# Kernel tuning notes

Measured on AMD Instinct MI355X. Metric: run time of the kernel, lower is better.

The kernel has to match this reference:

```python
import jax, jax.numpy as jnp
import numpy as np

N_NODES = 100000
N_EDGES = 6400000
N_ORDERS = 4
EPO = N_EDGES // N_ORDERS  # edges per order
K = 10


def setup_inputs() -> dict:
    key = jax.random.key(0)
    ks = jax.random.split(key, 7)
    x = jax.random.normal(ks[0], (N_NODES, K), dtype=jnp.float32)
    w_mp = jax.random.normal(ks[1], (K, 2 * K), dtype=jnp.float32) * (1.0 / np.sqrt(2 * K))
    b_mp = jax.random.normal(ks[2], (K,), dtype=jnp.float32) * 0.01
    w_out = jax.random.normal(ks[3], (K, K), dtype=jnp.float32) * (1.0 / np.sqrt(K))
    b_out = jax.random.normal(ks[4], (K,), dtype=jnp.float32) * 0.01
    edge_index = jax.random.randint(ks[5], (2, N_EDGES), 0, N_NODES, dtype=jnp.int64)
    orders = jax.random.randint(ks[6], (N_ORDERS, EPO), 0, N_EDGES, dtype=jnp.int64)
    return {"x": x, "w_mp": w_mp, "b_mp": b_mp, "w_out": w_out,
            "b_out": b_out, "edge_index": edge_index, "orders": orders}


def reference(x, w_mp, b_mp, w_out, b_out, edge_index, orders):
    n = x.shape[0]

    def step(h, order_idx):
        ei = edge_index[:, order_idx]            # [2, EPO] edges of this order
        # torch code swaps rows [1,0] before propagate, so in PyG terms:
        # source j = original row 1, target i = original row 0
        dst = ei[0]
        src = ei[1]
        x_i = h[dst]                             # [EPO, K]
        x_j = h[src]                             # [EPO, K]
        msg_in = jnp.concatenate([x_i, x_j - x_i], axis=1)   # [EPO, 2K]
        msg = msg_in @ w_mp.T + b_mp             # [EPO, K]
        aggr = jax.ops.segment_sum(msg, dst, num_segments=n)  # scatter-add
        return aggr + h, None                    # update(): aggr_out + x

    h, _ = jax.lax.scan(step, x, orders)
    return h @ w_out.T + b_out
```

## Files before the change

kernel.cpp:

```cpp
#include <hip/hip_runtime.h>

#define BLK 256
#define WBITS 13
#define W1CAP 9216
#define STCAP 4608
#define MAXNW 1024
#define MAXK2 2048
#define MAXNBD 512
#define OVFN 65536
#define IPTA 32
#define NSL 18
#define SENT 0xFFFFFFFFu

__global__ void k_init_h(const float* __restrict__ x, float* __restrict__ h, int n) {
    int total = n * 16;
    int gs = gridDim.x * blockDim.x;
    for (int i = blockIdx.x * blockDim.x + threadIdx.x; i < total; i += gs) {
        int row = i >> 4, col = i & 15;
        h[i] = (col < 10) ? x[row * 10 + col] : 0.0f;
    }
}

__global__ __launch_bounds__(512) void k_win(const int* __restrict__ orders,
                                             int total, int epo, int NW,
                                             int* __restrict__ gcnt1,
                                             unsigned* __restrict__ recs1,
                                             int* __restrict__ ovf1_cnt,
                                             unsigned* __restrict__ ovf1) {
    __shared__ int bcnt[MAXNW];
    __shared__ int gbase[MAXNW];
    int t = threadIdx.x;
    for (int i = t; i < NW; i += 512) bcnt[i] = 0;
    __syncthreads();

    size_t base = (size_t)blockIdx.x * (512 * IPTA);
    int st0 = (int)(base / (size_t)epo);
    size_t b1 = (size_t)(st0 + 1) * (size_t)epo;

    unsigned recr[IPTA]; int rr[IPTA];
    #pragma unroll
    for (int q = 0; q < IPTA; ++q) {
        size_t g = base + (size_t)q * 512 + t;
        recr[q] = SENT; rr[q] = 0;
        if (g < (size_t)total) {
            int idx = orders[g];
            int st = (g >= b1) ? (st0 + 1) : st0;
            recr[q] = ((unsigned)st << 23) | (unsigned)idx;
            rr[q] = atomicAdd(&bcnt[idx >> WBITS], 1);
        }
    }
    __syncthreads();
    for (int k = t; k < NW; k += 512) {
        int c = bcnt[k];
        gbase[k] = c ? atomicAdd(&gcnt1[k], c) : 0;
    }
    __syncthreads();
    #pragma unroll
    for (int q = 0; q < IPTA; ++q) {
        if (recr[q] != SENT) {
            int idx = (int)(recr[q] & 0x7FFFFFu);
            int key = idx >> WBITS;
            int pos = gbase[key] + rr[q];
            if (pos < W1CAP)
                recs1[(size_t)key * W1CAP + pos] = recr[q];
            else {
                int o = atomicAdd(ovf1_cnt, 1);
                if (o < OVFN) ovf1[o] = recr[q];
            }
        }
    }
}

__global__ __launch_bounds__(512) void k_bsort(const int* __restrict__ ei, int ne,
                                               const int* __restrict__ gcnt1,
                                               const unsigned* __restrict__ recs1,
                                               int NW, int NBD, int K2,
                                               unsigned* __restrict__ recs2,
                                               int* __restrict__ blk_offs) {
    __shared__ unsigned srt[W1CAP];
    __shared__ int cnt2[MAXK2];
    __shared__ int lofs[MAXK2 + 1];
    __shared__ int sc[512];
    int t = threadIdx.x;
    for (int i = t; i < K2; i += 512) cnt2[i] = 0;
    __syncthreads();

    int w = blockIdx.x;
    int c = gcnt1[w]; if (c > W1CAP) c = W1CAP;
    const unsigned* strm = recs1 + (size_t)w * W1CAP;

    int recr[NSL];
    #pragma unroll
    for (int q = 0; q < NSL; ++q) {
        int r = q * 512 + t;
        recr[q] = (r < c) ? (int)strm[r] : -1;
    }
    int dv[NSL];
    #pragma unroll
    for (int q = 0; q < NSL; ++q)
        dv[q] = (recr[q] >= 0) ? ei[recr[q] & 0x7FFFFF] : 0;
    unsigned meta[NSL];
    #pragma unroll
    for (int q = 0; q < NSL; ++q) {
        meta[q] = SENT;
        if (recr[q] >= 0) {
            int st = (int)(((unsigned)recr[q]) >> 23);
            int key = st * NBD + (dv[q] >> 8);
            int rk = atomicAdd(&cnt2[key], 1);
            meta[q] = ((unsigned)dv[q] << 14) | (unsigned)rk;
        }
    }
    __syncthreads();

    {
        int v[4]; int sum = 0;
        #pragma unroll
        for (int i = 0; i < 4; ++i) {
            int k = t * 4 + i;
            v[i] = (k < K2) ? cnt2[k] : 0;
            sum += v[i];
        }
        sc[t] = sum;
        __syncthreads();
        for (int off = 1; off < 512; off <<= 1) {
            int u = (t >= off) ? sc[t - off] : 0;
            __syncthreads();
            sc[t] += u;
            __syncthreads();
        }
        int run = sc[t] - sum;
        #pragma unroll
        for (int i = 0; i < 4; ++i) {
            int k = t * 4 + i;
            if (k <= K2) lofs[k] = run;
            run += v[i];
        }
        if (t == 511) lofs[K2] = sc[511];
    }
    __syncthreads();

    #pragma unroll
    for (int q = 0; q < NSL; ++q) {
        if (meta[q] != SENT) {
            int idx = recr[q] & 0x7FFFFF;
            int st  = (int)(((unsigned)recr[q]) >> 23);
            int s = ei[(size_t)ne + idx];
            int d = (int)(meta[q] >> 14);
            int rk = (int)(meta[q] & 0x3FFFu);
            int key = st * NBD + (d >> 8);
            srt[lofs[key] + rk] = ((unsigned)(d & 255) << 20) | (unsigned)s;
        }
    }
    __syncthreads();

    unsigned* dst = recs2 + (size_t)w * W1CAP;
    for (int r = t; r < c; r += 512) dst[r] = srt[r];
    int* bo = blk_offs + (size_t)w * (K2 + 1);
    for (int k = t; k <= K2; k += 512) bo[k] = lofs[k];
}

template<bool FINAL>
__global__ __launch_bounds__(512) void k_agg3(const float* __restrict__ h_cur,
                                              float* __restrict__ h_next,
                                              const int* __restrict__ blk_offs,
                                              const unsigned* __restrict__ recs2,
                                              int NW, int K2, int NBD, int st,
                                              const float* __restrict__ w_mp,
                                              const float* __restrict__ b_mp,
                                              const float* __restrict__ w_out,
                                              const float* __restrict__ b_out,
                                              float* __restrict__ out, int n,
                                              int* __restrict__ ovf2_cnt,
                                              int2* __restrict__ ovf2) {
    __shared__ unsigned stage[STCAP];
    __shared__ unsigned srt[STCAP];
    __shared__ int cnts[256];
    __shared__ int sc[256];
    __shared__ int offs[257];
    __shared__ int cursor;
    __shared__ float part[256 * 10];
    __shared__ float Wa[100], Wb[100], Bm[10];
    __shared__ float Wo[100], Bo[10];
    int t = threadIdx.x;
    if (t < 100) {
        int k = t / 10, j = t - k * 10;
        float w1 = w_mp[k * 20 + j];
        float w2 = w_mp[k * 20 + 10 + j];
        Wa[t] = w1 - w2; Wb[t] = w2;
        if (FINAL) Wo[t] = w_out[t];
    }
    if (t < 10) { Bm[t] = b_mp[t]; if (FINAL) Bo[t] = b_out[t]; }
    if (t < 256) cnts[t] = 0;
    if (t == 0) cursor = 0;
    __syncthreads();

    int bkt = blockIdx.x;
    int key = st * NBD + bkt;

    for (int b = t; b < NW; b += 512) {
        const int* bo = blk_offs + (size_t)b * (K2 + 1) + key;
        int o0 = bo[0], o1 = bo[1];
        int len = o1 - o0;
        if (len > 0) {
            int base = atomicAdd(&cursor, len);
            const unsigned* src = recs2 + (size_t)b * W1CAP + o0;
            for (int i = 0; i < len; ++i) {
                unsigned rec = src[i];
                int pos = base + i;
                if (pos < STCAP) {
                    stage[pos] = rec;
                    atomicAdd(&cnts[rec >> 20], 1);
                } else {
                    int o = atomicAdd(ovf2_cnt, 1);
                    if (o < OVFN)
                        ovf2[o] = make_int2((st << 18) | (bkt * 256 + (int)(rec >> 20)),
                                            (int)(rec & 0xFFFFFu));
                }
            }
        }
    }
    __syncthreads();
    int T = cursor; if (T > STCAP) T = STCAP;

    if (t < 256) sc[t] = cnts[t];
    __syncthreads();
    for (int off = 1; off < 256; off <<= 1) {
        int v = (t < 256 && t >= off) ? sc[t - off] : 0;
        __syncthreads();
        if (t < 256) sc[t] += v;
        __syncthreads();
    }
    if (t < 256) offs[t + 1] = sc[t];
    if (t == 0) offs[0] = 0;
    __syncthreads();
    if (t < 256) cnts[t] = offs[t];
    __syncthreads();

    for (int r = t; r < T; r += 512) {
        unsigned rec = stage[r];
        int pos = atomicAdd(&cnts[rec >> 20], 1);
        srt[pos] = rec;
    }
    __syncthreads();

    int node = t & 255, half = t >> 8;
    int b0 = offs[node], m = offs[node + 1] - b0;
    float S[10] = {0,0,0,0,0,0,0,0,0,0};
    for (int p = b0 + half; p < b0 + m; p += 2) {
        int s = (int)(srt[p] & 0xFFFFFu);
        const float* pj = h_cur + (size_t)s * 16;
        float4 a0 = *(const float4*)(pj);
        float4 a1 = *(const float4*)(pj + 4);
        float2 a2 = *(const float2*)(pj + 8);
        S[0] += a0.x; S[1] += a0.y; S[2] += a0.z; S[3] += a0.w;
        S[4] += a1.x; S[5] += a1.y; S[6] += a1.z; S[7] += a1.w;
        S[8] += a2.x; S[9] += a2.y;
    }
    if (half == 1) {
        #pragma unroll
        for (int j = 0; j < 10; ++j) part[node * 10 + j] = S[j];
    }
    __syncthreads();
    if (half == 0) {
        int i = bkt * 256 + node;
        if (i < n) {
            #pragma unroll
            for (int j = 0; j < 10; ++j) S[j] += part[node * 10 + j];
            const float* pi = h_cur + (size_t)i * 16;
            float4 x0 = *(const float4*)(pi);
            float4 x1 = *(const float4*)(pi + 4);
            float2 x2 = *(const float2*)(pi + 8);
            float xi[10] = {x0.x, x0.y, x0.z, x0.w, x1.x, x1.y, x1.z, x1.w, x2.x, x2.y};
            float deg = (float)m;
            float o[10];
            #pragma unroll
            for (int k = 0; k < 10; ++k) {
                float ma = Bm[k];
                float mb = 0.0f;
                #pragma unroll
                for (int j = 0; j < 10; ++j) {
                    ma += Wa[k * 10 + j] * xi[j];
                    mb += Wb[k * 10 + j] * S[j];
                }
                o[k] = xi[k] + deg * ma + mb;
            }
            if (FINAL) {
                float q2[10];
                #pragma unroll
                for (int k = 0; k < 10; ++k) {
                    float m2 = Bo[k];
                    #pragma unroll
                    for (int j = 0; j < 10; ++j) m2 += Wo[k * 10 + j] * o[j];
                    q2[k] = m2;
                }
                float* po = out + (size_t)i * 10;
                *(float2*)(po)     = make_float2(q2[0], q2[1]);
                *(float2*)(po + 2) = make_float2(q2[2], q2[3]);
                *(float2*)(po + 4) = make_float2(q2[4], q2[5]);
                *(float2*)(po + 6) = make_float2(q2[6], q2[7]);
                *(float2*)(po + 8) = make_float2(q2[8], q2[9]);
            } else {
                float* po = h_next + (size_t)i * 16;
                *(float4*)(po)     = make_float4(o[0], o[1], o[2], o[3]);
                *(float4*)(po + 4) = make_float4(o[4], o[5], o[6], o[7]);
                *(float2*)(po + 8) = make_float2(o[8], o[9]);
            }
        }
    }
}

__global__ void k_fix(const float* __restrict__ h_cur, float* __restrict__ h_next,
                      const int* __restrict__ ei, int ne,
                      const int* __restrict__ ovf1_cnt, const unsigned* __restrict__ ovf1,
                      const int* __restrict__ ovf2_cnt, const int2* __restrict__ ovf2,
                      const float* __restrict__ w_mp, const float* __restrict__ b_mp,
                      int st) {
    __shared__ float Wa[100], Wb[100], Bm[10];
    int t = threadIdx.x;
    if (t < 100) {
        int k = t / 10, j = t - k * 10;
        float w1 = w_mp[k * 20 + j];
        float w2 = w_mp[k * 20 + 10 + j];
        Wa[t] = w1 - w2; Wb[t] = w2;
    }
    if (t < 10) Bm[t] = b_mp[t];
    __syncthreads();
    int c1 = *ovf1_cnt; if (c1 > OVFN) c1 = OVFN;
    int c2 = *ovf2_cnt; if (c2 > OVFN) c2 = OVFN;
    int gs = gridDim.x * blockDim.x;
    for (int i = blockIdx.x * blockDim.x + t; i < c1 + c2; i += gs) {
        int d, s;
        if (i < c1) {
            unsigned v = ovf1[i];
            if ((int)(v >> 23) != st) continue;
            int idx = (int)(v & 0x7FFFFFu);
            d = ei[idx]; s = ei[(size_t)ne + idx];
        } else {
            int2 p = ovf2[i - c1];
            if ((p.x >> 18) != st) continue;
            d = p.x & 0x3FFFF; s = p.y;
        }
        const float* pi = h_cur + (size_t)d * 16;
        const float* pj = h_cur + (size_t)s * 16;
        float xi[10], xj[10];
        #pragma unroll
        for (int j = 0; j < 10; ++j) { xi[j] = pi[j]; xj[j] = pj[j]; }
        float* po = h_next + (size_t)d * 16;
        #pragma unroll
        for (int k = 0; k < 10; ++k) {
            float m = Bm[k];
            #pragma unroll
            for (int j = 0; j < 10; ++j) m += Wa[k * 10 + j] * xi[j] + Wb[k * 10 + j] * xj[j];
            atomicAdd(po + k, m);
        }
    }
}

__global__ void k_fix_final(const float* __restrict__ h_cur, float* __restrict__ out,
                            const int* __restrict__ ei, int ne,
                            const int* __restrict__ ovf1_cnt, const unsigned* __restrict__ ovf1,
                            const int* __restrict__ ovf2_cnt, const int2* __restrict__ ovf2,
                            const float* __restrict__ w_mp, const float* __restrict__ b_mp,
                            const float* __restrict__ w_out, int st) {
    __shared__ float Wa[100], Wb[100], Bm[10], Wo[100];
    int t = threadIdx.x;
    if (t < 100) {
        int k = t / 10, j = t - k * 10;
        float w1 = w_mp[k * 20 + j];
        float w2 = w_mp[k * 20 + 10 + j];
        Wa[t] = w1 - w2; Wb[t] = w2;
        Wo[t] = w_out[t];
    }
    if (t < 10) Bm[t] = b_mp[t];
    __syncthreads();
    int c1 = *ovf1_cnt; if (c1 > OVFN) c1 = OVFN;
    int c2 = *ovf2_cnt; if (c2 > OVFN) c2 = OVFN;
    int gs = gridDim.x * blockDim.x;
    for (int i = blockIdx.x * blockDim.x + t; i < c1 + c2; i += gs) {
        int d, s;
        if (i < c1) {
            unsigned v = ovf1[i];
            if ((int)(v >> 23) != st) continue;
            int idx = (int)(v & 0x7FFFFFu);
            d = ei[idx]; s = ei[(size_t)ne + idx];
        } else {
            int2 p = ovf2[i - c1];
            if ((p.x >> 18) != st) continue;
            d = p.x & 0x3FFFF; s = p.y;
        }
        const float* pi = h_cur + (size_t)d * 16;
        const float* pj = h_cur + (size_t)s * 16;
        float xi[10], xj[10];
        #pragma unroll
        for (int j = 0; j < 10; ++j) { xi[j] = pi[j]; xj[j] = pj[j]; }
        float dm[10];
        #pragma unroll
        for (int k = 0; k < 10; ++k) {
            float m = Bm[k];
            #pragma unroll
            for (int j = 0; j < 10; ++j) m += Wa[k * 10 + j] * xi[j] + Wb[k * 10 + j] * xj[j];
            dm[k] = m;
        }
        float* po = out + (size_t)d * 10;
        #pragma unroll
        for (int q = 0; q < 10; ++q) {
            float m = 0.0f;
            #pragma unroll
            for (int k = 0; k < 10; ++k) m += Wo[q * 10 + k] * dm[k];
            atomicAdd(po + q, m);
        }
    }
}


__global__ void k_init10(const float* __restrict__ x, float* __restrict__ h, int n10) {
    int gs = gridDim.x * blockDim.x;
    for (int i = blockIdx.x * blockDim.x + threadIdx.x; i < n10; i += gs) h[i] = x[i];
}
__global__ void k_copy4(const float4* __restrict__ src, float4* __restrict__ dst, int n4) {
    int gs = gridDim.x * blockDim.x;
    for (int i = blockIdx.x * blockDim.x + threadIdx.x; i < n4; i += gs) dst[i] = src[i];
}
__global__ void k_edge_step10(const float* __restrict__ h_cur, float* __restrict__ h_next,
                              const int* __restrict__ edge_index, const int* __restrict__ order,
                              const float* __restrict__ w_mp, const float* __restrict__ b_mp,
                              int epo, int ne) {
    __shared__ float Wc[200]; __shared__ float Bc[10];
    int t = threadIdx.x;
    if (t < 200) {
        int k = t / 20, j = t - k * 20;
        float w = w_mp[t];
        Wc[t] = (j < 10) ? (w - w_mp[k * 20 + j + 10]) : w;
    }
    if (t < 10) Bc[t] = b_mp[t];
    __syncthreads();
    int gs = gridDim.x * blockDim.x;
    for (int e = blockIdx.x * blockDim.x + t; e < epo; e += gs) {
        int idx = order[e];
        int dst = edge_index[idx];
        int src = edge_index[(size_t)ne + idx];
        const float* pi = h_cur + (size_t)dst * 10;
        const float* pj = h_cur + (size_t)src * 10;
        float xi[10], xj[10];
        #pragma unroll
        for (int j = 0; j < 10; ++j) { xi[j] = pi[j]; xj[j] = pj[j]; }
        float* po = h_next + (size_t)dst * 10;
        #pragma unroll
        for (int k = 0; k < 10; ++k) {
            float m = Bc[k];
            #pragma unroll
            for (int j = 0; j < 10; ++j) m += Wc[k * 20 + j] * xi[j] + Wc[k * 20 + 10 + j] * xj[j];
            atomicAdd(po + k, m);
        }
    }
}
__global__ void k_out10(const float* __restrict__ h, const float* __restrict__ w_out,
                        const float* __restrict__ b_out, float* __restrict__ out, int n) {
    __shared__ float W[100]; __shared__ float B[10];
    int t = threadIdx.x;
    if (t < 100) W[t] = w_out[t];
    if (t < 10)  B[t] = b_out[t];
    __syncthreads();
    int gs = gridDim.x * blockDim.x;
    for (int i = blockIdx.x * blockDim.x + t; i < n; i += gs) {
        float xi[10];
        #pragma unroll
        for (int j = 0; j < 10; ++j) xi[j] = h[(size_t)i * 10 + j];
        #pragma unroll
        for (int k = 0; k < 10; ++k) {
            float m = B[k];
            #pragma unroll
            for (int j = 0; j < 10; ++j) m += W[k * 10 + j] * xi[j];
            out[(size_t)i * 10 + k] = m;
        }
    }
}


extern "C" void kernel_launch(void* const* d_in, const int* in_sizes, int n_in,
                              void* d_out, int out_size, void* d_ws, size_t ws_size,
                              hipStream_t stream) {
    const float* x      = (const float*)d_in[0];
    const float* w_mp   = (const float*)d_in[1];
    const float* b_mp   = (const float*)d_in[2];
    const float* w_out  = (const float*)d_in[3];
    const float* b_out  = (const float*)d_in[4];
    const int*   edge_i = (const int*)d_in[5];
    const int*   orders = (const int*)d_in[6];

    int n  = in_sizes[0] / 10;
    int ne = in_sizes[5] / 2;
    const int n_orders = 4;
    int epo = in_sizes[6] / n_orders;
    int total = n_orders * epo;

    float* out = (float*)d_out;

    int NBD = (n + 255) >> 8;
    int NW  = (ne + (1 << WBITS) - 1) >> WBITS;
    int K2  = 4 * NBD;

    size_t off_hA    = 0;
    size_t off_hB    = off_hA + (size_t)n * 16;
    size_t off_recs1 = off_hB + (size_t)n * 16;
    size_t off_recs2 = off_recs1 + (size_t)NW * W1CAP;
    size_t off_boffs = off_recs2 + (size_t)NW * W1CAP;
    size_t off_ovf2  = off_boffs + (size_t)NW * (K2 + 1);
    if (off_ovf2 & 1) off_ovf2++;
    size_t off_ovf1  = off_ovf2 + (size_t)2 * OVFN;
    size_t off_gcnt1 = off_ovf1 + OVFN;
    size_t off_cnts  = off_gcnt1 + NW;
    size_t need      = (off_cnts + 2) * 4;

    bool ok = (ws_size >= need) && (NW <= MAXNW) && (NBD <= MAXNBD) &&
              (K2 <= MAXK2) && (ne <= (1 << 23)) && (n < (1 << 17));

    if (!ok) {
        float* hA = (float*)d_ws;
        float* hB = hA + (size_t)n * 10;
        int n10 = n * 10;
        hipLaunchKernelGGL(k_init10, dim3(min((n10 + BLK - 1) / BLK, 2048)), dim3(BLK), 0, stream,
                           x, hA, n10);
        int n4 = n10 / 4;
        float* cur = hA; float* nxt = hB;
        int gb_edge = min((epo + BLK - 1) / BLK, 6400);
        for (int s = 0; s < n_orders; ++s) {
            hipLaunchKernelGGL(k_copy4, dim3(min((n4 + BLK - 1) / BLK, 2048)), dim3(BLK), 0, stream,
                               (const float4*)cur, (float4*)nxt, n4);
            hipLaunchKernelGGL(k_edge_step10, dim3(gb_edge), dim3(BLK), 0, stream,
                               cur, nxt, edge_i, orders + (size_t)s * epo, w_mp, b_mp, epo, ne);
            float* t2 = cur; cur = nxt; nxt = t2;
        }
        hipLaunchKernelGGL(k_out10, dim3(min((n + BLK - 1) / BLK, 2048)), dim3(BLK), 0, stream,
                           cur, w_out, b_out, out, n);
        return;
    }

    float*    hA      = (float*)d_ws;
    float*    hB      = (float*)d_ws + off_hB;
    unsigned* recs1   = (unsigned*)d_ws + off_recs1;
    unsigned* recs2   = (unsigned*)d_ws + off_recs2;
    int*      boffs   = (int*)d_ws + off_boffs;
    int2*     ovf2    = (int2*)((int*)d_ws + off_ovf2);
    unsigned* ovf1    = (unsigned*)d_ws + off_ovf1;
    int*      gcnt1   = (int*)d_ws + off_gcnt1;
    int*      ovfcnts = (int*)d_ws + off_cnts;

    hipMemsetAsync(gcnt1, 0, ((size_t)NW + 2) * sizeof(int), stream);

    int gb_init = min((n * 16 + BLK - 1) / BLK, 2048);
    hipLaunchKernelGGL(k_init_h, dim3(gb_init), dim3(BLK), 0, stream, x, hA, n);

    int gbA = (total + 512 * IPTA - 1) / (512 * IPTA);
    hipLaunchKernelGGL(k_win, dim3(gbA), dim3(512), 0, stream,
                       orders, total, epo, NW, gcnt1, recs1, ovfcnts + 0, ovf1);

    hipLaunchKernelGGL(k_bsort, dim3(NW), dim3(512), 0, stream,
                       edge_i, ne, gcnt1, recs1, NW, NBD, K2, recs2, boffs);

    float* cur = hA; float* nxt = hB;
    for (int s = 0; s < n_orders; ++s) {
        bool fin = (s == n_orders - 1);
        if (fin) {
            hipLaunchKernelGGL((k_agg3<true>), dim3(NBD), dim3(512), 0, stream,
                               cur, nxt, boffs, recs2, NW, K2, NBD, s,
                               w_mp, b_mp, w_out, b_out, out, n,
                               ovfcnts + 1, ovf2);
            hipLaunchKernelGGL(k_fix_final, dim3(8), dim3(256), 0, stream,
                               cur, out, edge_i, ne,
                               ovfcnts + 0, ovf1, ovfcnts + 1, ovf2,
                               w_mp, b_mp, w_out, s);
        } else {
            hipLaunchKernelGGL((k_agg3<false>), dim3(NBD), dim3(512), 0, stream,
                               cur, nxt, boffs, recs2, NW, K2, NBD, s,
                               w_mp, b_mp, w_out, b_out, out, n,
                               ovfcnts + 1, ovf2);
            hipLaunchKernelGGL(k_fix, dim3(8), dim3(256), 0, stream,
                               cur, nxt, edge_i, ne,
                               ovfcnts + 0, ovf1, ovfcnts + 1, ovf2,
                               w_mp, b_mp, s);
            float* t2 = cur; cur = nxt; nxt = t2;
        }
    }
}
```

Baseline: 287.0 us.

## Replace global-atomic window binning with per-tile local sort and wave-parallel gather

The first binning pass now sorts each 8192-record tile by window in shared memory and writes contiguous runs plus per-tile offsets, replacing scattered writes driven by global atomics. The bucket-sort kernel gathers its window's runs from all tiles through a staging buffer. Both it and the aggregation kernel copy runs with whole wavefronts instead of one thread per run. This removes global atomic contention and serial per-thread copy loops, at the cost of an extra offset table and a gather stage.

```diff
diff --git a/kernel.cpp b/kernel.cpp
--- a/kernel.cpp
+++ b/kernel.cpp
@@ -2,14 +2,16 @@
 
 #define BLK 256
 #define WBITS 13
+#define TILEW 8192
+#define IPTW 16
 #define W1CAP 9216
+#define NSL 18
 #define STCAP 4608
 #define MAXNW 1024
+#define MAXNWB 1024
 #define MAXK2 2048
 #define MAXNBD 512
 #define OVFN 65536
-#define IPTA 32
-#define NSL 18
 #define SENT 0xFFFFFFFFu
 
 __global__ void k_init_h(const float* __restrict__ x, float* __restrict__ h, int n) {
@@ -21,79 +23,120 @@
     }
 }
 
-__global__ __launch_bounds__(512) void k_win(const int* __restrict__ orders,
-                                             int total, int epo, int NW,
-                                             int* __restrict__ gcnt1,
-                                             unsigned* __restrict__ recs1,
-                                             int* __restrict__ ovf1_cnt,
-                                             unsigned* __restrict__ ovf1) {
+__global__ __launch_bounds__(512) void k_win2(const int* __restrict__ orders,
+                                              int total, int epo, int NW,
+                                              unsigned* __restrict__ recs1,
+                                              int* __restrict__ woffs) {
+    __shared__ unsigned srt[TILEW];
     __shared__ int bcnt[MAXNW];
-    __shared__ int gbase[MAXNW];
+    __shared__ int lofs[MAXNW + 1];
+    __shared__ int sc[512];
     int t = threadIdx.x;
     for (int i = t; i < NW; i += 512) bcnt[i] = 0;
     __syncthreads();
 
-    size_t base = (size_t)blockIdx.x * (512 * IPTA);
+    int b = blockIdx.x;
+    size_t base = (size_t)b * TILEW;
+    int lim = (int)((size_t)total - base < TILEW ? (size_t)total - base : TILEW);
     int st0 = (int)(base / (size_t)epo);
-    size_t b1 = (size_t)(st0 + 1) * (size_t)epo;
-
-    unsigned recr[IPTA]; int rr[IPTA];
+    size_t bnd = (size_t)(st0 + 1) * (size_t)epo;
+
+    unsigned recr[IPTW]; int rr[IPTW];
     #pragma unroll
-    for (int q = 0; q < IPTA; ++q) {
-        size_t g = base + (size_t)q * 512 + t;
+    for (int q = 0; q < IPTW; ++q) {
+        int e = q * 512 + t;
         recr[q] = SENT; rr[q] = 0;
-        if (g < (size_t)total) {
+        if (e < lim) {
+            size_t g = base + e;
             int idx = orders[g];
-            int st = (g >= b1) ? (st0 + 1) : st0;
+            int st = (g >= bnd) ? (st0 + 1) : st0;
             recr[q] = ((unsigned)st << 23) | (unsigned)idx;
             rr[q] = atomicAdd(&bcnt[idx >> WBITS], 1);
         }
     }
     __syncthreads();
-    for (int k = t; k < NW; k += 512) {
-        int c = bcnt[k];
-        gbase[k] = c ? atomicAdd(&gcnt1[k], c) : 0;
+    {
+        int k0 = 2 * t;
+        int v0 = (k0 < NW) ? bcnt[k0] : 0;
+        int v1 = (k0 + 1 < NW) ? bcnt[k0 + 1] : 0;
+        int sum = v0 + v1;
+        sc[t] = sum;
+        __syncthreads();
+        for (int off = 1; off < 512; off <<= 1) {
+            int u = (t >= off) ? sc[t - off] : 0;
+            __syncthreads();
+            sc[t] += u;
+            __syncthreads();
+        }
+        int run = sc[t] - sum;
+        if (k0 <= NW) lofs[k0] = run;
+        if (k0 + 1 <= NW) lofs[k0 + 1] = run + v0;
     }
     __syncthreads();
     #pragma unroll
-    for (int q = 0; q < IPTA; ++q) {
+    for (int q = 0; q < IPTW; ++q) {
         if (recr[q] != SENT) {
             int idx = (int)(recr[q] & 0x7FFFFFu);
-            int key = idx >> WBITS;
-            int pos = gbase[key] + rr[q];
-            if (pos < W1CAP)
-                recs1[(size_t)key * W1CAP + pos] = recr[q];
-            else {
-                int o = atomicAdd(ovf1_cnt, 1);
-                if (o < OVFN) ovf1[o] = recr[q];
-            }
-        }
-    }
+            srt[lofs[idx >> WBITS] + rr[q]] = recr[q];
+        }
+    }
+    __syncthreads();
+    unsigned* dst = recs1 + base;
+    for (int r = t; r < lim; r += 512) dst[r] = srt[r];
+    int* bo = woffs + (size_t)b * (NW + 1);
+    for (int k = t; k <= NW; k += 512) bo[k] = lofs[k];
 }
 
 __global__ __launch_bounds__(512) void k_bsort(const int* __restrict__ ei, int ne,
-                                               const int* __restrict__ gcnt1,
                                                const unsigned* __restrict__ recs1,
-                                               int NW, int NBD, int K2,
+                                               const int* __restrict__ woffs,
+                                               int NWB, int NW, int NBD, int K2,
                                                unsigned* __restrict__ recs2,
-                                               int* __restrict__ blk_offs) {
-    __shared__ unsigned srt[W1CAP];
+                                               int* __restrict__ boffs,
+                                               int* __restrict__ ovf1_cnt,
+                                               unsigned* __restrict__ ovf1) {
+    __shared__ unsigned stage[W1CAP];
     __shared__ int cnt2[MAXK2];
     __shared__ int lofs[MAXK2 + 1];
     __shared__ int sc[512];
+    __shared__ int so0[MAXNWB];
+    __shared__ int slen[MAXNWB];
+    __shared__ int cursor;
     int t = threadIdx.x;
+    int w = blockIdx.x;
     for (int i = t; i < K2; i += 512) cnt2[i] = 0;
-    __syncthreads();
-
-    int w = blockIdx.x;
-    int c = gcnt1[w]; if (c > W1CAP) c = W1CAP;
-    const unsigned* strm = recs1 + (size_t)w * W1CAP;
+    if (t == 0) cursor = 0;
+    for (int b = t; b < NWB; b += 512) {
+        const int* bo = woffs + (size_t)b * (NW + 1) + w;
+        int o0 = bo[0];
+        so0[b] = o0;
+        slen[b] = bo[1] - o0;
+    }
+    __syncthreads();
+
+    int lane = t & 63, wid = t >> 6;
+    for (int b = wid; b < NWB; b += 8) {
+        int len = slen[b];
+        if (len > 0) {
+            int bs = 0;
+            if (lane == 0) bs = atomicAdd(&cursor, len);
+            bs = __shfl(bs, 0);
+            const unsigned* src = recs1 + (size_t)b * TILEW + so0[b];
+            for (int i = lane; i < len; i += 64) {
+                int pos = bs + i;
+                if (pos < W1CAP) stage[pos] = src[i];
+                else { int o = atomicAdd(ovf1_cnt, 1); if (o < OVFN) ovf1[o] = src[i]; }
+            }
+        }
+    }
+    __syncthreads();
+    int T = cursor; if (T > W1CAP) T = W1CAP;
 
     int recr[NSL];
     #pragma unroll
     for (int q = 0; q < NSL; ++q) {
         int r = q * 512 + t;
-        recr[q] = (r < c) ? (int)strm[r] : -1;
+        recr[q] = (r < T) ? (int)stage[r] : -1;
     }
     int dv[NSL];
     #pragma unroll
@@ -111,7 +154,6 @@
         }
     }
     __syncthreads();
-
     {
         int v[4]; int sum = 0;
         #pragma unroll
@@ -138,7 +180,6 @@
         if (t == 511) lofs[K2] = sc[511];
     }
     __syncthreads();
-
     #pragma unroll
     for (int q = 0; q < NSL; ++q) {
         if (meta[q] != SENT) {
@@ -148,21 +189,20 @@
             int d = (int)(meta[q] >> 14);
             int rk = (int)(meta[q] & 0x3FFFu);
             int key = st * NBD + (d >> 8);
-            srt[lofs[key] + rk] = ((unsigned)(d & 255) << 20) | (unsigned)s;
-        }
-    }
-    __syncthreads();
-
+            stage[lofs[key] + rk] = ((unsigned)(d & 255) << 20) | (unsigned)s;
+        }
+    }
+    __syncthreads();
     unsigned* dst = recs2 + (size_t)w * W1CAP;
-    for (int r = t; r < c; r += 512) dst[r] = srt[r];
-    int* bo = blk_offs + (size_t)w * (K2 + 1);
-    for (int k = t; k <= K2; k += 512) bo[k] = lofs[k];
+    for (int r = t; r < T; r += 512) dst[r] = stage[r];
+    int* bo2 = boffs + (size_t)w * (K2 + 1);
+    for (int k = t; k <= K2; k += 512) bo2[k] = lofs[k];
 }
 
 template<bool FINAL>
 __global__ __launch_bounds__(512) void k_agg3(const float* __restrict__ h_cur,
                                               float* __restrict__ h_next,
-                                              const int* __restrict__ blk_offs,
+                                              const int* __restrict__ boffs,
                                               const unsigned* __restrict__ recs2,
                                               int NW, int K2, int NBD, int st,
                                               const float* __restrict__ w_mp,
@@ -174,6 +214,8 @@
                                               int2* __restrict__ ovf2) {
     __shared__ unsigned stage[STCAP];
     __shared__ unsigned srt[STCAP];
+    __shared__ int so0[MAXNW];
+    __shared__ int slen[MAXNW];
     __shared__ int cnts[256];
     __shared__ int sc[256];
     __shared__ int offs[257];
@@ -192,21 +234,27 @@
     if (t < 10) { Bm[t] = b_mp[t]; if (FINAL) Bo[t] = b_out[t]; }
     if (t < 256) cnts[t] = 0;
     if (t == 0) cursor = 0;
-    __syncthreads();
-
     int bkt = blockIdx.x;
     int key = st * NBD + bkt;
-
     for (int b = t; b < NW; b += 512) {
-        const int* bo = blk_offs + (size_t)b * (K2 + 1) + key;
-        int o0 = bo[0], o1 = bo[1];
-        int len = o1 - o0;
+        const int* bo = boffs + (size_t)b * (K2 + 1) + key;
+        int o0 = bo[0];
+        so0[b] = o0;
+        slen[b] = bo[1] - o0;
+    }
+    __syncthreads();
+
+    int lane = t & 63, wid = t >> 6;
+    for (int b = wid; b < NW; b += 8) {
+        int len = slen[b];
         if (len > 0) {
-            int base = atomicAdd(&cursor, len);
-            const unsigned* src = recs2 + (size_t)b * W1CAP + o0;
-            for (int i = 0; i < len; ++i) {
+            int bs = 0;
+            if (lane == 0) bs = atomicAdd(&cursor, len);
+            bs = __shfl(bs, 0);
+            const unsigned* src = recs2 + (size_t)b * W1CAP + so0[b];
+            for (int i = lane; i < len; i += 64) {
                 unsigned rec = src[i];
-                int pos = base + i;
+                int pos = bs + i;
                 if (pos < STCAP) {
                     stage[pos] = rec;
                     atomicAdd(&cnts[rec >> 20], 1);
@@ -499,21 +547,22 @@
     int NBD = (n + 255) >> 8;
     int NW  = (ne + (1 << WBITS) - 1) >> WBITS;
     int K2  = 4 * NBD;
+    int NWB = (total + TILEW - 1) / TILEW;
 
     size_t off_hA    = 0;
     size_t off_hB    = off_hA + (size_t)n * 16;
     size_t off_recs1 = off_hB + (size_t)n * 16;
-    size_t off_recs2 = off_recs1 + (size_t)NW * W1CAP;
+    size_t off_woffs = off_recs1 + (size_t)NWB * TILEW;
+    size_t off_recs2 = off_woffs + (size_t)NWB * (NW + 1);
     size_t off_boffs = off_recs2 + (size_t)NW * W1CAP;
     size_t off_ovf2  = off_boffs + (size_t)NW * (K2 + 1);
     if (off_ovf2 & 1) off_ovf2++;
     size_t off_ovf1  = off_ovf2 + (size_t)2 * OVFN;
-    size_t off_gcnt1 = off_ovf1 + OVFN;
-    size_t off_cnts  = off_gcnt1 + NW;
+    size_t off_cnts  = off_ovf1 + OVFN;
     size_t need      = (off_cnts + 2) * 4;
 
-    bool ok = (ws_size >= need) && (NW <= MAXNW) && (NBD <= MAXNBD) &&
-              (K2 <= MAXK2) && (ne <= (1 << 23)) && (n < (1 << 17));
+    bool ok = (ws_size >= need) && (NW <= MAXNW) && (NWB <= MAXNWB) &&
+              (NBD <= MAXNBD) && (K2 <= MAXK2) && (ne <= (1 << 23)) && (n < (1 << 17));
 
     if (!ok) {
         float* hA = (float*)d_ws;
@@ -539,24 +588,24 @@
     float*    hA      = (float*)d_ws;
     float*    hB      = (float*)d_ws + off_hB;
     unsigned* recs1   = (unsigned*)d_ws + off_recs1;
+    int*      woffs   = (int*)d_ws + off_woffs;
     unsigned* recs2   = (unsigned*)d_ws + off_recs2;
     int*      boffs   = (int*)d_ws + off_boffs;
     int2*     ovf2    = (int2*)((int*)d_ws + off_ovf2);
     unsigned* ovf1    = (unsigned*)d_ws + off_ovf1;
-    int*      gcnt1   = (int*)d_ws + off_gcnt1;
     int*      ovfcnts = (int*)d_ws + off_cnts;
 
-    hipMemsetAsync(gcnt1, 0, ((size_t)NW + 2) * sizeof(int), stream);
+    hipMemsetAsync(ovfcnts, 0, 2 * sizeof(int), stream);
 
     int gb_init = min((n * 16 + BLK - 1) / BLK, 2048);
     hipLaunchKernelGGL(k_init_h, dim3(gb_init), dim3(BLK), 0, stream, x, hA, n);
 
-    int gbA = (total + 512 * IPTA - 1) / (512 * IPTA);
-    hipLaunchKernelGGL(k_win, dim3(gbA), dim3(512), 0, stream,
-                       orders, total, epo, NW, gcnt1, recs1, ovfcnts + 0, ovf1);
+    hipLaunchKernelGGL(k_win2, dim3(NWB), dim3(512), 0, stream,
+                       orders, total, epo, NW, recs1, woffs);
 
     hipLaunchKernelGGL(k_bsort, dim3(NW), dim3(512), 0, stream,
-                       edge_i, ne, gcnt1, recs1, NW, NBD, K2, recs2, boffs);
+                       edge_i, ne, recs1, woffs, NWB, NW, NBD, K2,
+                       recs2, boffs, ovfcnts + 0, ovf1);
 
     float* cur = hA; float* nxt = hB;
     for (int s = 0; s < n_orders; ++s) {
```

After: 498.8 us. 73.8% more time.
